# Performance work log

Hardware: AMD Instinct MI355X
Metric: run time of the kernel (lower is better)

The kernel has to match this reference:

```python
import jax, jax.numpy as jnp
import numpy as np

jax.config.update("jax_enable_x64", True)  # int64 coordinate hashes (scaling up to 1e15)

N_IN, N_OUT = 64, 32
NP_, NG = 200000, 400000

# Same coordinate hash as the original module: columns [batch, x, y, z]
_SCALE = jnp.array([1, 10 ** 5, 10 ** 10, 10 ** 15], dtype=jnp.int64)
# 27 kernel offsets of the 3x3x3 generative transpose conv (output-stride units)
_OFF3 = np.array([[i, j, k] for i in (-1, 0, 1) for j in (-1, 0, 1) for k in (-1, 0, 1)], dtype=np.int64)
_OFF4 = jnp.asarray(np.concatenate([np.zeros((27, 1), np.int64), _OFF3], axis=1))  # batch offset = 0


def _hash(c):
    return (c.astype(jnp.int64) * _SCALE).sum(-1)


def setup_inputs() -> dict:
    rng = np.random.default_rng(0)
    G = 128  # stride-2 lattice: input coords are even, in [0, 256)
    lin = rng.choice(G ** 3, size=NP_, replace=False)  # unique voxels
    xs, ys, zs = lin % G, (lin // G) % G, lin // (G * G)
    in_coords = np.stack([np.zeros(NP_, np.int64), 2 * xs, 2 * ys, 2 * zs], axis=1)
    # guide (occupied) coords: input coords shifted by random kernel offsets -> mostly hits
    guide_coords = np.concatenate([in_coords, in_coords], axis=0).copy()
    guide_coords[:, 1:] += _OFF3[rng.integers(0, 27, size=NG)]
    key = jax.random.key(0)
    k1, k2, k3 = jax.random.split(key, 3)
    in_feats = jax.random.normal(k1, (NP_, N_IN), dtype=jnp.float32)
    weights = (jax.random.normal(k2, (27, N_IN, N_OUT), dtype=jnp.float32) / float(np.sqrt(27 * N_IN))).astype(jnp.float32)
    bias = (jax.random.normal(k3, (N_OUT,), dtype=jnp.float32) * 0.01).astype(jnp.float32)
    return {"in_feats": in_feats, "weights": weights, "bias": bias,
            "in_coords": jnp.asarray(in_coords), "guide_coords": jnp.asarray(guide_coords)}


def _forward(in_feats, weights, bias, in_coords, guide_coords):
    # Hash-table over input coordinates (sort + binary search == isin with index)
    in_keys = _hash(in_coords)                # [Np]
    order = jnp.argsort(in_keys)
    skeys = in_keys[order]
    n = skeys.shape[0]
    # Generative transpose conv: output q gets contribution from input p when q = p + off,
    # i.e. p = q - off. Pruning keeps only outputs coinciding with guide coords, so we
    # evaluate the conv directly at the guide coordinates and mask non-generated rows.
    p_keys = _hash(guide_coords[None, :, :] - _OFF4[:, None, :])   # [27, Ng]
    pos = jnp.clip(jnp.searchsorted(skeys, p_keys), 0, n - 1)
    found = skeys[pos] == p_keys                                   # [27, Ng] bool
    idx = order[pos]                                               # [27, Ng]

    def step(acc, xs):
        i, f, w = xs
        g = in_feats[i] * f[:, None].astype(in_feats.dtype)        # [Ng, N_in] gather + mask
        return acc + g @ w, None                                   # small GEMM per offset

    acc0 = jnp.zeros((guide_coords.shape[0], weights.shape[-1]), in_feats.dtype)
    acc, _ = jax.lax.scan(step, acc0, (idx, found, weights))
    exists = found.any(axis=0)                                     # generated-set membership
    return (acc + bias.astype(acc.dtype)) * exists[:, None].astype(acc.dtype)


def reference(in_feats, weights, bias, in_coords, guide_coords):
    return _forward(in_feats, weights, bias, in_coords, guide_coords)
```

## Files before the change

kernel.cpp:

```cpp
#include <hip/hip_runtime.h>

#define NIN 64
#define NOUT 32
#define TBITS 21
#define TSIZE (1 << TBITS)
#define NB 512
#define CHUNK 4096
#define KPT (CHUNK / 256)
#define BLKG 128

typedef __attribute__((ext_vector_type(8))) short short8;
typedef __attribute__((ext_vector_type(4))) float float4v;
typedef __attribute__((ext_vector_type(4))) unsigned short ushort4v;

__device__ __forceinline__ unsigned short bf16rne(float x) {
    unsigned u = __float_as_uint(x);
    u += 0x7fffu + ((u >> 16) & 1u);
    return (unsigned short)(u >> 16);
}

constexpr int popc8(int x) { int n = 0; for (int i = 0; i < 8; ++i) n += (x >> i) & 1; return n; }
constexpr int nth_sub(int C, int r) {
    int cnt = 0;
    for (int s = 0; s < 8; ++s)
        if ((s & ~C & 7) == 0) { if (cnt == r) return s; ++cnt; }
    return 0;
}

__device__ __forceinline__ int bucket_of(int4 q, int* cls) {
    int c = (q.y & 1) | ((q.z & 1) << 1) | ((q.w & 1) << 2);
    *cls = c;
    int sp = ((q.y >> 6) & 3) | (((q.z >> 6) & 3) << 2) | (((q.w >> 6) & 3) << 4);
    return (c << 6) | sp;
}

__global__ void prep(int4* __restrict__ ws4, int n4,
                     const float* __restrict__ w, unsigned short* __restrict__ wt,
                     const float* __restrict__ f, unsigned short* __restrict__ fb,
                     int fn4,
                     const int* __restrict__ guide, int ng, int* __restrict__ count) {
    __shared__ int hist[NB];
    int i = blockIdx.x * blockDim.x + threadIdx.x;
    if (i < n4) ws4[i] = make_int4(-1, -1, -1, -1);
    if (i < 27 * 64 * 32) {
        int oi = i >> 11;
        int k  = (i >> 5) & 63;
        int ch = i & 31;
        wt[oi * 2048 + ch * 64 + k] = bf16rne(w[i]);
    }
    if (i < fn4) {
        float4 v = ((const float4*)f)[i];
        ushort4v o;
        o.x = bf16rne(v.x); o.y = bf16rne(v.y);
        o.z = bf16rne(v.z); o.w = bf16rne(v.w);
        ((ushort4v*)fb)[i] = o;
    }
    int base = blockIdx.x * CHUNK;
    if (base < ng) {
        for (int j = threadIdx.x; j < NB; j += 256) hist[j] = 0;
        __syncthreads();
        int end = base + CHUNK; if (end > ng) end = ng;
        for (int j = base + threadIdx.x; j < end; j += 256) {
            int c;
            int b = bucket_of(((const int4*)guide)[j], &c);
            atomicAdd(&hist[b], 1);
        }
        __syncthreads();
        for (int j = threadIdx.x; j < NB; j += 256)
            if (hist[j]) atomicAdd(&count[j], hist[j]);
    }
}

__global__ void scanB(const int* __restrict__ count, int* __restrict__ cursor,
                      int* __restrict__ classbase) {
    __shared__ int ps[512];
    __shared__ int cb[9];
    int t = threadIdx.x;
    int v = count[t];
    ps[t] = v;
    __syncthreads();
    #pragma unroll
    for (int off = 1; off < 512; off <<= 1) {
        int val = ps[t];
        int u = (t >= off) ? ps[t - off] : 0;
        __syncthreads();
        ps[t] = val + u;
        __syncthreads();
    }
    int incl = ps[t];
    if (t == 0) {
        int base = 0;
        #pragma unroll
        for (int cc = 0; cc < 8; ++cc) {
            cb[cc] = base;
            int hi = ps[cc * 64 + 63];
            int lo = cc ? ps[cc * 64 - 1] : 0;
            base += (hi - lo + BLKG - 1) & ~(BLKG - 1);
        }
        cb[8] = base;
        for (int j = 0; j < 9; ++j) classbase[j] = cb[j];
    }
    __syncthreads();
    int cc = t >> 6;
    int lo = cc ? ps[cc * 64 - 1] : 0;
    cursor[t] = cb[cc] + (incl - v) - lo;
}

__global__ void scat(const int* __restrict__ coords, int np, int* __restrict__ table,
                     const int* __restrict__ guide, int ng,
                     int* __restrict__ cursor, int2* __restrict__ sorted) {
    int gi = blockIdx.x * blockDim.x + threadIdx.x;
    if (gi < np) {
        int x = coords[gi * 4 + 1];
        int y = coords[gi * 4 + 2];
        int z = coords[gi * 4 + 3];
        table[(x >> 1) | ((y >> 1) << 7) | ((z >> 1) << 14)] = gi;
    }
    __shared__ int hist[NB];
    int t = threadIdx.x;
    int base = blockIdx.x * CHUNK;
    if (base >= ng) return;
    for (int i = t; i < NB; i += 256) hist[i] = 0;
    __syncthreads();
    int packed[KPT];
    int ey[KPT];
    #pragma unroll
    for (int k = 0; k < KPT; ++k) {
        int i = base + k * 256 + t;
        packed[k] = -1;
        ey[k] = 0;
        if (i < ng) {
            int4 q = ((const int4*)guide)[i];
            int c;
            int b = bucket_of(q, &c);
            int lr = atomicAdd(&hist[b], 1);
            packed[k] = (b << 13) | lr;
            ey[k] = (q.y + 1) | ((q.z + 1) << 9) | ((q.w + 1) << 18);
        }
    }
    __syncthreads();
    for (int i = t; i < NB; i += 256) {
        int h = hist[i];
        hist[i] = h ? atomicAdd(&cursor[i], h) : 0;
    }
    __syncthreads();
    #pragma unroll
    for (int k = 0; k < KPT; ++k) {
        if (packed[k] >= 0) {
            int b  = packed[k] >> 13;
            int lr = packed[k] & 8191;
            int i  = base + k * 256 + t;
            int2 e;
            e.x = i | ((b >> 6) << 24);
            e.y = ey[k];
            sorted[hist[b] + lr] = e;
        }
    }
}


template<int C>
__device__ __forceinline__ void probe2t(const int* __restrict__ table, int2 s2,
                                        int quad, int* o0, int* o1) {
    int qx = (s2.y & 511) - 1;
    int qy = ((s2.y >> 9) & 511) - 1;
    int qz = ((s2.y >> 18) & 511) - 1;
    int res[2];
    #pragma unroll
    for (int r = 0; r < 2; ++r) {
        int sub = quad + r * 4;
        int offx = (C & 1) ? ((sub & 1) ? 1 : -1) : 0;
        int offy = (C & 2) ? ((sub & 2) ? 1 : -1) : 0;
        int offz = (C & 4) ? ((sub & 4) ? 1 : -1) : 0;
        int px = qx - offx, py = qy - offy, pz = qz - offz;
        bool valid = (s2.x >= 0) & ((sub & ~C & 7) == 0) &
                     ((unsigned)px < 256u) & ((unsigned)py < 256u) & ((unsigned)pz < 256u);
        int lin = (px >> 1) | ((py >> 1) << 7) | ((pz >> 1) << 14);
        int v = table[valid ? lin : 0];
        res[r] = valid ? v : -1;
    }
    *o0 = res[0]; *o1 = res[1];
}

template<int C, int R, int NS>
__device__ __forceinline__ void stage_rank(const unsigned short* __restrict__ wt,
                                           unsigned short* bshr, int mm, int jj) {
    if constexpr (R < NS) {
        constexpr int SUB = nth_sub(C, R);
        constexpr int offx = (C & 1) ? ((SUB & 1) ? 1 : -1) : 0;
        constexpr int offy = (C & 2) ? ((SUB & 2) ? 1 : -1) : 0;
        constexpr int offz = (C & 4) ? ((SUB & 4) ? 1 : -1) : 0;
        constexpr int oi = (offx + 1) * 9 + (offy + 1) * 3 + (offz + 1);
        short8 v = *(const short8*)(wt + oi * 2048 + mm * 64 + jj * 8);
        *(short8*)((char*)bshr + (R & 3) * 4096 + mm * 128 + ((jj ^ (mm & 7)) << 4)) = v;
    }
}

template<int USEFB, int C, int R, int NS>
__device__ __forceinline__ void rank_load(const float* __restrict__ feats,
                                          const unsigned short* __restrict__ fb,
                                          int idx0, int idx1,
                                          unsigned long long bal0, unsigned long long bal1,
                                          int m, int quad, short8* A0, short8* A1) {
    if constexpr (R < NS) {
        constexpr int SUB = nth_sub(C, R);
        unsigned long long bal = (SUB < 4) ? bal0 : bal1;
        unsigned rowm = (unsigned)((bal >> ((SUB & 3) * 16)) & 0xffffull);
        short8 z = {0,0,0,0,0,0,0,0};
        A0[R & 3] = z; A1[R & 3] = z;
        if (rowm) {
            int h = __shfl((SUB < 4) ? idx0 : idx1, (SUB & 3) * 16 + m, 64);
            if (h >= 0) {
                if constexpr (USEFB) {
                    const unsigned short* fp = fb + (size_t)h * NIN + quad * 8;
                    A0[R & 3] = *(const short8*)fp;
                    A1[R & 3] = *(const short8*)(fp + 32);
                } else {
                    const float4* fp = (const float4*)(feats + (size_t)h * NIN + quad * 8);
                    float4 fA = fp[0], fB = fp[1];
                    const float4* fp2 = (const float4*)(feats + (size_t)h * NIN + 32 + quad * 8);
                    float4 fC = fp2[0], fD = fp2[1];
                    short8 x, y;
                    x[0] = (short)bf16rne(fA.x); x[1] = (short)bf16rne(fA.y);
                    x[2] = (short)bf16rne(fA.z); x[3] = (short)bf16rne(fA.w);
                    x[4] = (short)bf16rne(fB.x); x[5] = (short)bf16rne(fB.y);
                    x[6] = (short)bf16rne(fB.z); x[7] = (short)bf16rne(fB.w);
                    y[0] = (short)bf16rne(fC.x); y[1] = (short)bf16rne(fC.y);
                    y[2] = (short)bf16rne(fC.z); y[3] = (short)bf16rne(fC.w);
                    y[4] = (short)bf16rne(fD.x); y[5] = (short)bf16rne(fD.y);
                    y[6] = (short)bf16rne(fD.z); y[7] = (short)bf16rne(fD.w);
                    A0[R & 3] = x; A1[R & 3] = y;
                }
            }
        }
    }
}

template<int C, int R, int NS>
__device__ __forceinline__ void rank_mm(const unsigned short* bshr,
                                        unsigned long long bal0, unsigned long long bal1,
                                        int m, int quad, const short8* A0, const short8* A1,
                                        float4v* acc0, float4v* acc1) {
    if constexpr (R < NS) {
        constexpr int SUB = nth_sub(C, R);
        unsigned long long bal = (SUB < 4) ? bal0 : bal1;
        unsigned rowm = (unsigned)((bal >> ((SUB & 3) * 16)) & 0xffffull);
        if (rowm) {
            const char* base = (const char*)bshr + (R & 3) * 4096;
            short8 b00 = *(const short8*)(base + m * 128 + ((quad ^ (m & 7)) << 4));
            short8 b10 = *(const short8*)(base + m * 128 + (((4 + quad) ^ (m & 7)) << 4));
            short8 b01 = *(const short8*)(base + (16 + m) * 128 + ((quad ^ ((16 + m) & 7)) << 4));
            short8 b11 = *(const short8*)(base + (16 + m) * 128 + (((4 + quad) ^ ((16 + m) & 7)) << 4));
            *acc0 = __builtin_amdgcn_mfma_f32_16x16x32_bf16(b00, A0[R & 3], *acc0, 0, 0, 0);
            *acc0 = __builtin_amdgcn_mfma_f32_16x16x32_bf16(b10, A1[R & 3], *acc0, 0, 0, 0);
            *acc1 = __builtin_amdgcn_mfma_f32_16x16x32_bf16(b01, A0[R & 3], *acc1, 0, 0, 0);
            *acc1 = __builtin_amdgcn_mfma_f32_16x16x32_bf16(b11, A1[R & 3], *acc1, 0, 0, 0);
        }
    }
}

template<int USEFB, int C, int P>
__device__ __forceinline__ void phase_tile(const float* __restrict__ feats,
                                           const unsigned short* __restrict__ fb,
                                           const unsigned short* bshr,
                                           int idx0, int idx1,
                                           unsigned long long bal0, unsigned long long bal1,
                                           int m, int quad, float4v* acc0, float4v* acc1) {
    constexpr int NS = 1 << popc8(C);
    short8 A0[4], A1[4];
    rank_load<USEFB, C, P * 4 + 0, NS>(feats, fb, idx0, idx1, bal0, bal1, m, quad, A0, A1);
    rank_load<USEFB, C, P * 4 + 1, NS>(feats, fb, idx0, idx1, bal0, bal1, m, quad, A0, A1);
    rank_load<USEFB, C, P * 4 + 2, NS>(feats, fb, idx0, idx1, bal0, bal1, m, quad, A0, A1);
    rank_load<USEFB, C, P * 4 + 3, NS>(feats, fb, idx0, idx1, bal0, bal1, m, quad, A0, A1);
    rank_mm<C, P * 4 + 0, NS>(bshr, bal0, bal1, m, quad, A0, A1, acc0, acc1);
    rank_mm<C, P * 4 + 1, NS>(bshr, bal0, bal1, m, quad, A0, A1, acc0, acc1);
    rank_mm<C, P * 4 + 2, NS>(bshr, bal0, bal1, m, quad, A0, A1, acc0, acc1);
    rank_mm<C, P * 4 + 3, NS>(bshr, bal0, bal1, m, quad, A0, A1, acc0, acc1);
}

__device__ __forceinline__ void store_tile(int2 s2, unsigned long long eb,
                                           float4v acc0, float4v acc1,
                                           int m, int quad, const float* __restrict__ bias,
                                           float* __restrict__ out) {
    int id = (s2.x < 0) ? -1 : (s2.x & 0xffffff);
    if (id < 0) return;
    unsigned e16 = (unsigned)((eb | (eb >> 16) | (eb >> 32) | (eb >> 48)) & 0xffffull);
    bool ex = (e16 >> m) & 1;
    float4 b0 = ((const float4*)bias)[quad];
    float4 b1 = ((const float4*)bias)[4 + quad];
    float4v v0, v1;
    v0[0] = ex ? (acc0[0] + b0.x) : 0.f;
    v0[1] = ex ? (acc0[1] + b0.y) : 0.f;
    v0[2] = ex ? (acc0[2] + b0.z) : 0.f;
    v0[3] = ex ? (acc0[3] + b0.w) : 0.f;
    v1[0] = ex ? (acc1[0] + b1.x) : 0.f;
    v1[1] = ex ? (acc1[1] + b1.y) : 0.f;
    v1[2] = ex ? (acc1[2] + b1.z) : 0.f;
    v1[3] = ex ? (acc1[3] + b1.w) : 0.f;
    float* op = out + (size_t)id * NOUT;
    *(float4v*)(op + quad * 4)      = v0;
    *(float4v*)(op + 16 + quad * 4) = v1;
}

template<int USEFB, int C>
__device__ __forceinline__ void conv_class(const float* __restrict__ feats,
                                           const unsigned short* __restrict__ fb,
                                           const float* __restrict__ bias,
                                           const int* __restrict__ table,
                                           const int2* __restrict__ sorted,
                                           const unsigned short* __restrict__ wt,
                                           float* __restrict__ out,
                                           int bt0, unsigned short* bshr) {
    constexpr int NS = 1 << popc8(C);
    int tid = threadIdx.x;
    int wid = tid >> 6, lane = tid & 63;
    int m = lane & 15, quad = lane >> 4;

    int t0 = bt0 + wid * 2;
    int2 s2a = sorted[t0 * 16 + m];
    int2 s2b = sorted[t0 * 16 + 16 + m];
    int ia0, ia1, ib0, ib1;
    probe2t<C>(table, s2a, quad, &ia0, &ia1);
    probe2t<C>(table, s2b, quad, &ib0, &ib1);

    {
        int mm = tid >> 3, jj = tid & 7;
        stage_rank<C, 0, NS>(wt, bshr, mm, jj);
        stage_rank<C, 1, NS>(wt, bshr, mm, jj);
        stage_rank<C, 2, NS>(wt, bshr, mm, jj);
        stage_rank<C, 3, NS>(wt, bshr, mm, jj);
    }
    __syncthreads();

    unsigned long long balA0 = __ballot(ia0 >= 0), balA1 = __ballot(ia1 >= 0);
    unsigned long long balB0 = __ballot(ib0 >= 0), balB1 = __ballot(ib1 >= 0);

    float4v aA0 = {0.f,0.f,0.f,0.f}, aA1 = {0.f,0.f,0.f,0.f};
    float4v aB0 = {0.f,0.f,0.f,0.f}, aB1 = {0.f,0.f,0.f,0.f};

    phase_tile<USEFB, C, 0>(feats, fb, bshr, ia0, ia1, balA0, balA1, m, quad, &aA0, &aA1);
    phase_tile<USEFB, C, 0>(feats, fb, bshr, ib0, ib1, balB0, balB1, m, quad, &aB0, &aB1);

    if constexpr (NS > 4) {
        __syncthreads();
        {
            int mm = tid >> 3, jj = tid & 7;
            stage_rank<C, 4, NS>(wt, bshr, mm, jj);
            stage_rank<C, 5, NS>(wt, bshr, mm, jj);
            stage_rank<C, 6, NS>(wt, bshr, mm, jj);
            stage_rank<C, 7, NS>(wt, bshr, mm, jj);
        }
        __syncthreads();
        phase_tile<USEFB, C, 1>(feats, fb, bshr, ia0, ia1, balA0, balA1, m, quad, &aA0, &aA1);
        phase_tile<USEFB, C, 1>(feats, fb, bshr, ib0, ib1, balB0, balB1, m, quad, &aB0, &aB1);
    }

    store_tile(s2a, balA0 | balA1, aA0, aA1, m, quad, bias, out);
    store_tile(s2b, balB0 | balB1, aB0, aB1, m, quad, bias, out);
}

template<int USEFB>
__launch_bounds__(256, 6)
__global__ void gen_conv(const float* __restrict__ feats,
                         const unsigned short* __restrict__ fb,
                         const float* __restrict__ bias,
                         const int* __restrict__ table,
                         const int2* __restrict__ sorted,
                         const int* __restrict__ classbase,
                         const unsigned short* __restrict__ wt,
                         float* __restrict__ out) {
    __shared__ unsigned short bshr[8192];

    int nwg = gridDim.x;
    int orig = blockIdx.x;
    int qd = nwg >> 3, rd = nwg & 7;
    int xc = orig & 7, ix = orig >> 3;
    int wg = (xc < rd ? xc * (qd + 1) : rd * (qd + 1) + (xc - rd) * qd) + ix;

    int g0 = wg * BLKG;
    if (g0 >= classbase[8]) return;
    int c = 0;
    #pragma unroll
    for (int j = 1; j < 8; ++j) c += (g0 >= classbase[j]) ? 1 : 0;
    c = __builtin_amdgcn_readfirstlane(c);
    int bt0 = wg * (BLKG / 16);

    switch (c) {
        case 0: conv_class<USEFB, 0>(feats, fb, bias, table, sorted, wt, out, bt0, bshr); break;
        case 1: conv_class<USEFB, 1>(feats, fb, bias, table, sorted, wt, out, bt0, bshr); break;
        case 2: conv_class<USEFB, 2>(feats, fb, bias, table, sorted, wt, out, bt0, bshr); break;
        case 3: conv_class<USEFB, 3>(feats, fb, bias, table, sorted, wt, out, bt0, bshr); break;
        case 4: conv_class<USEFB, 4>(feats, fb, bias, table, sorted, wt, out, bt0, bshr); break;
        case 5: conv_class<USEFB, 5>(feats, fb, bias, table, sorted, wt, out, bt0, bshr); break;
        case 6: conv_class<USEFB, 6>(feats, fb, bias, table, sorted, wt, out, bt0, bshr); break;
        case 7: conv_class<USEFB, 7>(feats, fb, bias, table, sorted, wt, out, bt0, bshr); break;
    }
}

extern "C" void kernel_launch(void* const* d_in, const int* in_sizes, int n_in,
                              void* d_out, int out_size, void* d_ws, size_t ws_size,
                              hipStream_t stream) {
    const float* feats   = (const float*)d_in[0];
    const float* weights = (const float*)d_in[1];
    const float* bias    = (const float*)d_in[2];
    const int*   coords  = (const int*)d_in[3];
    const int*   guide   = (const int*)d_in[4];
    float* out = (float*)d_out;

    int np = in_sizes[3] / 4;
    int ng = in_sizes[4] / 4;

    int* wsI = (int*)d_ws;
    int SC = (ng + 8 * BLKG + 3) & ~3;
    int A = TSIZE + 2 * SC;
    int* table     = wsI;
    int2* sorted   = (int2*)(wsI + TSIZE);
    int* count     = wsI + A;
    int* cursor    = wsI + A + 512;
    int* classbase = wsI + A + 1024;
    unsigned short* wt = (unsigned short*)(wsI + A + 1040);
    unsigned short* fb = (unsigned short*)(wsI + A + 1040 + 27648);
    size_t need = ((size_t)A + 1040 + 27648) * 4 + (size_t)np * NIN * 2;
    int usefb = (ws_size >= need) ? 1 : 0;

    hipMemsetAsync(count, 0, NB * sizeof(int), stream);

    int n4 = A / 4;
    int fn4 = usefb ? np * (NIN / 4) : 0;
    int prep_n = n4 > fn4 ? n4 : fn4;
    if (prep_n < 27 * 64 * 32) prep_n = 27 * 64 * 32;
    int prep_blocks = (prep_n + 255) / 256;
    int cblocks = (ng + CHUNK - 1) / CHUNK;
    if (prep_blocks < cblocks) prep_blocks = cblocks;
    hipLaunchKernelGGL(prep, dim3(prep_blocks), dim3(256), 0, stream,
                       (int4*)wsI, n4, weights, wt, feats, fb, fn4, guide, ng, count);

    hipLaunchKernelGGL(scanB, dim3(1), dim3(512), 0, stream, count, cursor, classbase);

    int sb1 = (np + 255) / 256;
    int sblocks = sb1 > cblocks ? sb1 : cblocks;
    hipLaunchKernelGGL(scat, dim3(sblocks), dim3(256), 0, stream,
                       coords, np, table, guide, ng, cursor, sorted);

    int maxguides = ng + 8 * (BLKG - 1);
    int blocks = (maxguides + BLKG - 1) / BLKG;
    if (usefb) {
        hipLaunchKernelGGL((gen_conv<1>), dim3(blocks), dim3(256), 0, stream,
                           feats, fb, bias, table, sorted, classbase, wt, out);
    } else {
        hipLaunchKernelGGL((gen_conv<0>), dim3(blocks), dim3(256), 0, stream,
                           feats, fb, bias, table, sorted, classbase, wt, out);
    }
}
```

Before: 170.8 us.

## Use per-chunk histograms for a deterministic spatial-major bucket sort

Bucket order becomes spatial-block major with parity class minor, and each bucket is padded to a BLKG multiple. Conv workgroups then cover spatially local guides and read their class from the first sorted entry. Global atomic cursors and the memset are replaced by per-chunk histograms plus a serial per-bucket exclusive scan, which gives deterministic, stable ordering. The costs are padding up to 512 buckets (more empty rows and more launched workgroups), a scan kernel that loops over ~98 chunks per thread, and a larger workspace.

```diff
diff --git a/kernel.cpp b/kernel.cpp
--- a/kernel.cpp
+++ b/kernel.cpp
@@ -31,14 +31,14 @@
     int c = (q.y & 1) | ((q.z & 1) << 1) | ((q.w & 1) << 2);
     *cls = c;
     int sp = ((q.y >> 6) & 3) | (((q.z >> 6) & 3) << 2) | (((q.w >> 6) & 3) << 4);
-    return (c << 6) | sp;
+    return (sp << 3) | c;
 }
 
 __global__ void prep(int4* __restrict__ ws4, int n4,
                      const float* __restrict__ w, unsigned short* __restrict__ wt,
                      const float* __restrict__ f, unsigned short* __restrict__ fb,
                      int fn4,
-                     const int* __restrict__ guide, int ng, int* __restrict__ count) {
+                     const int* __restrict__ guide, int ng, int* __restrict__ chunkhist) {
     __shared__ int hist[NB];
     int i = blockIdx.x * blockDim.x + threadIdx.x;
     if (i < n4) ws4[i] = make_int4(-1, -1, -1, -1);
@@ -67,48 +67,38 @@
         }
         __syncthreads();
         for (int j = threadIdx.x; j < NB; j += 256)
-            if (hist[j]) atomicAdd(&count[j], hist[j]);
-    }
-}
-
-__global__ void scanB(const int* __restrict__ count, int* __restrict__ cursor,
-                      int* __restrict__ classbase) {
-    __shared__ int ps[512];
-    __shared__ int cb[9];
+            chunkhist[blockIdx.x * NB + j] = hist[j];
+    }
+}
+
+__global__ void scanB(int* __restrict__ chunkhist, int cblocks, int* __restrict__ total) {
+    __shared__ int ps[NB];
     int t = threadIdx.x;
-    int v = count[t];
-    ps[t] = v;
+    int cnt = 0;
+    for (int ch = 0; ch < cblocks; ++ch) cnt += chunkhist[ch * NB + t];
+    int padded = (cnt + BLKG - 1) & ~(BLKG - 1);
+    ps[t] = padded;
     __syncthreads();
     #pragma unroll
-    for (int off = 1; off < 512; off <<= 1) {
-        int val = ps[t];
+    for (int off = 1; off < NB; off <<= 1) {
+        int v = ps[t];
         int u = (t >= off) ? ps[t - off] : 0;
         __syncthreads();
-        ps[t] = val + u;
-        __syncthreads();
-    }
-    int incl = ps[t];
-    if (t == 0) {
-        int base = 0;
-        #pragma unroll
-        for (int cc = 0; cc < 8; ++cc) {
-            cb[cc] = base;
-            int hi = ps[cc * 64 + 63];
-            int lo = cc ? ps[cc * 64 - 1] : 0;
-            base += (hi - lo + BLKG - 1) & ~(BLKG - 1);
-        }
-        cb[8] = base;
-        for (int j = 0; j < 9; ++j) classbase[j] = cb[j];
-    }
-    __syncthreads();
-    int cc = t >> 6;
-    int lo = cc ? ps[cc * 64 - 1] : 0;
-    cursor[t] = cb[cc] + (incl - v) - lo;
+        ps[t] = v + u;
+        __syncthreads();
+    }
+    if (t == NB - 1) total[0] = ps[NB - 1];
+    int run = ps[t] - padded;
+    for (int ch = 0; ch < cblocks; ++ch) {
+        int v = chunkhist[ch * NB + t];
+        chunkhist[ch * NB + t] = run;
+        run += v;
+    }
 }
 
 __global__ void scat(const int* __restrict__ coords, int np, int* __restrict__ table,
                      const int* __restrict__ guide, int ng,
-                     int* __restrict__ cursor, int2* __restrict__ sorted) {
+                     const int* __restrict__ chunkhist, int2* __restrict__ sorted) {
     int gi = blockIdx.x * blockDim.x + threadIdx.x;
     if (gi < np) {
         int x = coords[gi * 4 + 1];
@@ -139,10 +129,8 @@
         }
     }
     __syncthreads();
-    for (int i = t; i < NB; i += 256) {
-        int h = hist[i];
-        hist[i] = h ? atomicAdd(&cursor[i], h) : 0;
-    }
+    for (int i = t; i < NB; i += 256)
+        hist[i] = chunkhist[blockIdx.x * NB + i];
     __syncthreads();
     #pragma unroll
     for (int k = 0; k < KPT; ++k) {
@@ -151,7 +139,7 @@
             int lr = packed[k] & 8191;
             int i  = base + k * 256 + t;
             int2 e;
-            e.x = i | ((b >> 6) << 24);
+            e.x = i | ((b & 7) << 24);
             e.y = ey[k];
             sorted[hist[b] + lr] = e;
         }
@@ -366,7 +354,7 @@
                          const float* __restrict__ bias,
                          const int* __restrict__ table,
                          const int2* __restrict__ sorted,
-                         const int* __restrict__ classbase,
+                         const int* __restrict__ totalp,
                          const unsigned short* __restrict__ wt,
                          float* __restrict__ out) {
     __shared__ unsigned short bshr[8192];
@@ -378,10 +366,8 @@
     int wg = (xc < rd ? xc * (qd + 1) : rd * (qd + 1) + (xc - rd) * qd) + ix;
 
     int g0 = wg * BLKG;
-    if (g0 >= classbase[8]) return;
-    int c = 0;
-    #pragma unroll
-    for (int j = 1; j < 8; ++j) c += (g0 >= classbase[j]) ? 1 : 0;
+    if (g0 >= totalp[0]) return;
+    int c = (sorted[g0].x >> 24) & 7;
     c = __builtin_amdgcn_readfirstlane(c);
     int bt0 = wg * (BLKG / 16);
 
@@ -410,45 +396,43 @@
     int np = in_sizes[3] / 4;
     int ng = in_sizes[4] / 4;
 
+    int cblocks = (ng + CHUNK - 1) / CHUNK;
     int* wsI = (int*)d_ws;
-    int SC = (ng + 8 * BLKG + 3) & ~3;
+    int SC = (ng + NB * BLKG + 3) & ~3;
     int A = TSIZE + 2 * SC;
     int* table     = wsI;
     int2* sorted   = (int2*)(wsI + TSIZE);
-    int* count     = wsI + A;
-    int* cursor    = wsI + A + 512;
-    int* classbase = wsI + A + 1024;
-    unsigned short* wt = (unsigned short*)(wsI + A + 1040);
-    unsigned short* fb = (unsigned short*)(wsI + A + 1040 + 27648);
-    size_t need = ((size_t)A + 1040 + 27648) * 4 + (size_t)np * NIN * 2;
+    int* total     = wsI + A;
+    int* chunkhist = wsI + A + 4;
+    int CH = cblocks * NB;
+    unsigned short* wt = (unsigned short*)(wsI + A + 4 + CH);
+    unsigned short* fb = (unsigned short*)(wsI + A + 4 + CH + 27648);
+    size_t need = ((size_t)A + 4 + CH + 27648) * 4 + (size_t)np * NIN * 2;
     int usefb = (ws_size >= need) ? 1 : 0;
-
-    hipMemsetAsync(count, 0, NB * sizeof(int), stream);
 
     int n4 = A / 4;
     int fn4 = usefb ? np * (NIN / 4) : 0;
     int prep_n = n4 > fn4 ? n4 : fn4;
     if (prep_n < 27 * 64 * 32) prep_n = 27 * 64 * 32;
     int prep_blocks = (prep_n + 255) / 256;
-    int cblocks = (ng + CHUNK - 1) / CHUNK;
     if (prep_blocks < cblocks) prep_blocks = cblocks;
     hipLaunchKernelGGL(prep, dim3(prep_blocks), dim3(256), 0, stream,
-                       (int4*)wsI, n4, weights, wt, feats, fb, fn4, guide, ng, count);
-
-    hipLaunchKernelGGL(scanB, dim3(1), dim3(512), 0, stream, count, cursor, classbase);
+                       (int4*)wsI, n4, weights, wt, feats, fb, fn4, guide, ng, chunkhist);
+
+    hipLaunchKernelGGL(scanB, dim3(1), dim3(NB), 0, stream, chunkhist, cblocks, total);
 
     int sb1 = (np + 255) / 256;
     int sblocks = sb1 > cblocks ? sb1 : cblocks;
     hipLaunchKernelGGL(scat, dim3(sblocks), dim3(256), 0, stream,
-                       coords, np, table, guide, ng, cursor, sorted);
-
-    int maxguides = ng + 8 * (BLKG - 1);
+                       coords, np, table, guide, ng, chunkhist, sorted);
+
+    int maxguides = ng + NB * (BLKG - 1);
     int blocks = (maxguides + BLKG - 1) / BLKG;
     if (usefb) {
         hipLaunchKernelGGL((gen_conv<1>), dim3(blocks), dim3(256), 0, stream,
-                           feats, fb, bias, table, sorted, classbase, wt, out);
+                           feats, fb, bias, table, sorted, total, wt, out);
     } else {
         hipLaunchKernelGGL((gen_conv<0>), dim3(blocks), dim3(256), 0, stream,
-                           feats, fb, bias, table, sorted, classbase, wt, out);
-    }
-}
+                           feats, fb, bias, table, sorted, total, wt, out);
+    }
+}
```

After: 184.6 us. 1.08x slower.
